# Kernel optimization log

Measured on AMD Instinct MI355X. Metric: run time of the kernel, lower is better.

The kernel has to match this reference:

```python
import jax, jax.numpy as jnp
import numpy as np
import math

B, T, C, H = 2, 2048, 768, 12
HD = C // H
EPS = 1e-5

def setup_inputs() -> dict:
    key = jax.random.key(0)
    ks = jax.random.split(key, 12)
    s = lambda n: 1.0 / math.sqrt(n)
    return {
        "x": jax.random.normal(ks[0], (B, T, C), jnp.float32),
        "ln1_g": jnp.ones((C,), jnp.float32),
        "ln1_b": jnp.zeros((C,), jnp.float32),
        "w_attn": jax.random.normal(ks[1], (C, 3 * C), jnp.float32) * s(C),
        "b_attn": jnp.zeros((3 * C,), jnp.float32),
        "w_proj": jax.random.normal(ks[2], (C, C), jnp.float32) * s(C),
        "b_proj": jnp.zeros((C,), jnp.float32),
        "ln2_g": jnp.ones((C,), jnp.float32),
        "ln2_b": jnp.zeros((C,), jnp.float32),
        "w_fc": jax.random.normal(ks[3], (C, 4 * C), jnp.float32) * s(C),
        "b_fc": jnp.zeros((4 * C,), jnp.float32),
        "w_fc2": jax.random.normal(ks[4], (4 * C, C), jnp.float32) * s(4 * C),
        "b_fc2": jnp.zeros((C,), jnp.float32),
    }

def layernorm(x, g, b):
    mu = jnp.mean(x, axis=-1, keepdims=True)
    var = jnp.mean(jnp.square(x - mu), axis=-1, keepdims=True)
    return (x - mu) * jax.lax.rsqrt(var + EPS) * g + b

def new_gelu(x):
    c = math.sqrt(2.0 / math.pi)
    return 0.5 * x * (1.0 + jnp.tanh(c * (x + 0.044715 * x ** 3)))

def reference(x, ln1_g, ln1_b, w_attn, b_attn, w_proj, b_proj,
              ln2_g, ln2_b, w_fc, b_fc, w_fc2, b_fc2):
    # --- attention branch ---
    h = layernorm(x, ln1_g, ln1_b)
    qkv = h @ w_attn + b_attn                       # [B,T,3C]
    q, k, v = jnp.split(qkv, 3, axis=-1)
    q = q.reshape(B, T, H, HD).transpose(0, 2, 1, 3)  # [B,H,T,hd]
    k = k.reshape(B, T, H, HD).transpose(0, 2, 1, 3)
    v = v.reshape(B, T, H, HD).transpose(0, 2, 1, 3)
    att = jnp.einsum('bhqd,bhkd->bhqk', q, k) * (1.0 / math.sqrt(HD))
    causal = jnp.tril(jnp.ones((T, T), bool))
    att = jnp.where(causal, att, -jnp.inf)
    att = jax.nn.softmax(att, axis=-1)
    y = jnp.einsum('bhqk,bhkd->bhqd', att, v)       # [B,H,T,hd]
    y = y.transpose(0, 2, 1, 3).reshape(B, T, C)
    x = x + y @ w_proj + b_proj
    # --- MLP branch ---
    h2 = layernorm(x, ln2_g, ln2_b)
    x = x + new_gelu(h2 @ w_fc + b_fc) @ w_fc2 + b_fc2
    return x
```

## Files before the change

kernel.cpp:

```cpp
#include <hip/hip_runtime.h>
#include <hip/hip_bf16.h>
#include <math.h>

typedef __hip_bfloat16 bf16;
typedef __attribute__((ext_vector_type(8))) short short8;
typedef __attribute__((ext_vector_type(4))) float floatx4;
typedef __attribute__((ext_vector_type(4))) unsigned uintx4;

#define GLDS16(g, l) __builtin_amdgcn_global_load_lds( \
    (const __attribute__((address_space(1))) void*)(g), \
    (__attribute__((address_space(3))) void*)(l), 16, 0, 0)

__device__ __forceinline__ bf16 f2bf(float v) { return __float2bfloat16(v); }

__device__ __forceinline__ unsigned cvtpk(float a, float b) {
  unsigned r;
  asm volatile("v_cvt_pk_bf16_f32 %0, %1, %2" : "=v"(r) : "v"(a), "v"(b));
  return r;
}

__global__ __launch_bounds__(256) void kconvT(const float* __restrict__ w,
                                              bf16* __restrict__ wT,
                                              int K, int N) {
  __shared__ float tile[32][33];
  const int n0 = blockIdx.x * 32, k0 = blockIdx.y * 32;
  const int tc = threadIdx.x & 31, tr = threadIdx.x >> 5;
#pragma unroll
  for (int p = 0; p < 4; p++)
    tile[tr + p * 8][tc] = w[(size_t)(k0 + tr + p * 8) * N + n0 + tc];
  __syncthreads();
#pragma unroll
  for (int p = 0; p < 4; p++)
    wT[(size_t)(n0 + tr + p * 8) * K + k0 + tc] = f2bf(tile[tc][tr + p * 8]);
}

__global__ __launch_bounds__(256) void kln(const float* __restrict__ x,
                                           const float* __restrict__ gw,
                                           const float* __restrict__ bw,
                                           bf16* __restrict__ out) {
  const int row = blockIdx.x, tid = threadIdx.x;
  const float* xr = x + (size_t)row * 768;
  float v0 = xr[tid], v1 = xr[tid + 256], v2 = xr[tid + 512];
  float s = v0 + v1 + v2;
  float s2 = v0 * v0 + v1 * v1 + v2 * v2;
#pragma unroll
  for (int off = 1; off < 64; off <<= 1) {
    s += __shfl_xor(s, off);
    s2 += __shfl_xor(s2, off);
  }
  __shared__ float red[8];
  const int wid = tid >> 6, lane = tid & 63;
  if (lane == 0) { red[wid] = s; red[4 + wid] = s2; }
  __syncthreads();
  s = red[0] + red[1] + red[2] + red[3];
  s2 = red[4] + red[5] + red[6] + red[7];
  const float mu = s * (1.f / 768.f);
  const float rst = rsqrtf(fmaxf(s2 * (1.f / 768.f) - mu * mu, 0.f) + 1e-5f);
  bf16* orow = out + (size_t)row * 768;
  orow[tid] = f2bf((v0 - mu) * rst * gw[tid] + bw[tid]);
  orow[tid + 256] = f2bf((v1 - mu) * rst * gw[tid + 256] + bw[tid + 256]);
  orow[tid + 512] = f2bf((v2 - mu) * rst * gw[tid + 512] + bw[tid + 512]);
}

__global__ __launch_bounds__(256) void kxpose(const bf16* __restrict__ qkv,
                                              bf16* __restrict__ VT) {
  const int T = 2048, C3 = 2304;
  const int t0 = blockIdx.x * 64, h = blockIdx.y, b = blockIdx.z;
  const int tid = threadIdx.x;
  __shared__ short tile[64][66];
  const bf16* src = qkv + (size_t)b * T * C3 + 1536 + h * 64;
  const int tr = tid >> 3, c = tid & 7;
#pragma unroll
  for (int p = 0; p < 2; p++) {
    short8 v = *(const short8*)(src + (size_t)(t0 + tr + p * 32) * C3 + c * 8);
    *(short8*)&tile[tr + p * 32][c * 8] = v;
  }
  __syncthreads();
  bf16* dst = VT + ((size_t)(b * 12 + h) * 64) * T + t0;
#pragma unroll
  for (int p = 0; p < 2; p++) {
    const int d = (tid >> 3) + p * 32, tc = tid & 7;
    short8 v;
#pragma unroll
    for (int j = 0; j < 8; j++) v[j] = tile[tc * 8 + j][d];
    *(short8*)(dst + (size_t)d * T + tc * 8) = v;
  }
}

template <int BN, int EPI>
__global__ __launch_bounds__(256, 2) void kgemm(
    const bf16* __restrict__ A, const bf16* __restrict__ BT,
    const float* __restrict__ bias, const float* __restrict__ resid,
    bf16* __restrict__ outb, float* __restrict__ outf, int M, int N, int K,
    int NXB) {
  __shared__ bf16 As[3][128 * 32];
  __shared__ bf16 Bs[3][BN * 32];
  const int tid = threadIdx.x;
  const int wid = tid >> 6, lane = tid & 63, g = lane >> 4, q = lane & 15;
  constexpr int FM = (BN == 128) ? 4 : 2;
  constexpr int FN = 4;
  constexpr int WM = (BN == 128) ? 64 : 32;
  const int wr = (BN == 128) ? (wid >> 1) : wid;
  const int wc = (BN == 128) ? (wid & 1) : 0;

  const int bid = blockIdx.x;
  const int lb = (bid & 7) * ((int)gridDim.x >> 3) + (bid >> 3);
  const int row0 = (lb / NXB) * 128, col0 = (lb % NXB) * BN;

  floatx4 acc[FM][FN] = {};
  const int r0 = tid >> 2;
  const int c0 = (((tid & 3) ^ ((r0 >> 1) & 3))) * 8;
  const int lsl = (g ^ ((q >> 1) & 3)) * 16;
  const bf16* Ab = A + (size_t)row0 * K;
  const bf16* Bb = BT + (size_t)col0 * K;

  auto STAGE = [&](int kk, int buf) {
    GLDS16(Ab + (size_t)r0 * K + kk + c0, (char*)&As[buf][0] + wid * 1024);
    GLDS16(Ab + (size_t)(r0 + 64) * K + kk + c0,
           (char*)&As[buf][0] + 4096 + wid * 1024);
    GLDS16(Bb + (size_t)r0 * K + kk + c0, (char*)&Bs[buf][0] + wid * 1024);
    if constexpr (BN == 128)
      GLDS16(Bb + (size_t)(r0 + 64) * K + kk + c0,
             (char*)&Bs[buf][0] + 4096 + wid * 1024);
  };

  const int nk = K >> 5;
  STAGE(0, 0);
  STAGE(32, 1);

  for (int kt = 0; kt < nk; kt++) {
    if (kt + 2 < nk) {
      STAGE((kt + 2) << 5, (kt + 2) % 3);
      if constexpr (BN == 128) asm volatile("s_waitcnt vmcnt(8)");
      else asm volatile("s_waitcnt vmcnt(6)");
    } else if (kt + 1 < nk) {
      if constexpr (BN == 128) asm volatile("s_waitcnt vmcnt(4)");
      else asm volatile("s_waitcnt vmcnt(3)");
    } else {
      asm volatile("s_waitcnt vmcnt(0)");
    }
    __syncthreads();

    const char* Ac = (const char*)&As[kt % 3][0];
    const char* Bc = (const char*)&Bs[kt % 3][0];
    short8 af[FM], bfr[FN];
#pragma unroll
    for (int m = 0; m < FM; m++)
      af[m] = *(const short8*)(Ac + (wr * WM + m * 16 + q) * 64 + lsl);
#pragma unroll
    for (int n = 0; n < FN; n++)
      bfr[n] = *(const short8*)(Bc + (wc * 64 + n * 16 + q) * 64 + lsl);
#pragma unroll
    for (int m = 0; m < FM; m++)
#pragma unroll
      for (int n = 0; n < FN; n++)
        acc[m][n] =
            __builtin_amdgcn_mfma_f32_16x16x32_bf16(af[m], bfr[n], acc[m][n], 0, 0, 0);
    __syncthreads();
  }

#pragma unroll
  for (int n = 0; n < FN; n++) {
    const int col = col0 + wc * 64 + n * 16 + q;
    const float bv = bias[col];
#pragma unroll
    for (int m = 0; m < FM; m++) {
      const int rowb = row0 + wr * WM + m * 16 + g * 4;
#pragma unroll
      for (int r = 0; r < 4; r++) {
        const size_t idx = (size_t)(rowb + r) * N + col;
        const float v = acc[m][n][r] + bv;
        if (EPI == 0) {
          outb[idx] = f2bf(v);
        } else if (EPI == 1) {
          outf[idx] = v + resid[idx];
        } else {
          const float t = tanhf(0.7978845608028654f * (v + 0.044715f * v * v * v));
          outb[idx] = f2bf(0.5f * v * (1.0f + t));
        }
      }
    }
  }
}

__global__ __launch_bounds__(256, 2) void kattn(const bf16* __restrict__ qkv,
                                                const bf16* __restrict__ VT,
                                                bf16* __restrict__ y) {
  const int T = 2048, C3 = 2304;
  const int tid = threadIdx.x;
  const int w = tid >> 6, lane = tid & 63;
  const int g = lane >> 4, qi = lane & 15;

  const int bid = blockIdx.x;
  const int lb = (bid & 7) * 96 + (bid >> 3);
  const int qblk = 31 - (lb & 31);
  const int h = (lb >> 5) % 12, b = (lb >> 5) / 12;
  const int q0w = qblk * 64 + w * 16;
  const int qrow = q0w + qi;

  const bf16* Qb = qkv + (size_t)b * T * C3 + h * 64;
  const char* Ksrc = (const char*)(Qb + 768);
  const char* Vsrc = (const char*)(VT + (size_t)(b * 12 + h) * 64 * T);

  __shared__ __align__(16) char smem[32768];

  const int nt = qblk + 1;

  short8 qf[2];
#pragma unroll
  for (int s = 0; s < 2; s++)
    qf[s] = *(const short8*)(Qb + (size_t)qrow * C3 + s * 32 + g * 8);

  const int kvb = (qi >> 2) * 8 + (qi & 3);
  const unsigned swz = (unsigned)(((lane & 7) ^ (lane >> 3)) << 4);
  const int srow = lane >> 3;

  float m_run = -1e30f, l_run = 0.f;
  floatx4 o[4] = {};

#define STAGE(t)                                                                   \
  {                                                                                \
    char* base_ = smem + ((t) & 1) * 16384;                                        \
    const int kv0_ = (t) * 64;                                                     \
    _Pragma("unroll")                                                              \
    for (int j = 0; j < 2; j++) {                                                  \
      const int c_ = w * 2 + j;                                                    \
      GLDS16(Ksrc + (size_t)(kv0_ + c_ * 8 + srow) * 4608 + swz, base_ + c_ * 1024); \
      GLDS16(Vsrc + (size_t)(c_ * 8 + srow) * 4096 + kv0_ * 2 + swz,               \
             base_ + 8192 + c_ * 1024);                                            \
    }                                                                              \
  }

  STAGE(0);
  asm volatile("s_waitcnt vmcnt(0)");
  __syncthreads();

  for (int t = 0; t < nt; t++) {
    if (t + 1 < nt) STAGE(t + 1);
    const char* Kl = smem + (t & 1) * 16384;
    const char* Vl = Kl + 8192;
    const int kv0 = t * 64;

    short8 kf[8];
#pragma unroll
    for (int c = 0; c < 4; c++) {
      const int R = kvb + (c & 1) * 4 + (c >> 1) * 32;
#pragma unroll
      for (int s = 0; s < 2; s++)
        kf[c * 2 + s] =
            *(const short8*)(Kl + R * 128 + (((s * 4 + g) ^ (R & 7)) << 4));
    }
    short8 vfr[8];
#pragma unroll
    for (int ks = 0; ks < 2; ks++)
#pragma unroll
      for (int n = 0; n < 4; n++) {
        const int R2 = n * 16 + qi;
        vfr[ks * 4 + n] =
            *(const short8*)(Vl + R2 * 128 + (((ks * 4 + g) ^ (R2 & 7)) << 4));
      }

    floatx4 sacc[4] = {};
#pragma unroll
    for (int c = 0; c < 4; c++)
#pragma unroll
      for (int s = 0; s < 2; s++)
        sacc[c] =
            __builtin_amdgcn_mfma_f32_16x16x32_bf16(kf[c * 2 + s], qf[s], sacc[c], 0, 0, 0);

    if (kv0 + 63 > q0w) {
#pragma unroll
      for (int c = 0; c < 4; c++)
#pragma unroll
        for (int r = 0; r < 4; r++) {
          const int kv = kv0 + g * 8 + (c & 1) * 4 + r + (c >> 1) * 32;
          if (kv > qrow) sacc[c][r] = -1e30f;
        }
    }
    float mx = sacc[0][0];
#pragma unroll
    for (int c = 0; c < 4; c++)
#pragma unroll
      for (int r = 0; r < 4; r++) mx = fmaxf(mx, sacc[c][r]);
    mx = fmaxf(mx, __shfl_xor(mx, 16));
    mx = fmaxf(mx, __shfl_xor(mx, 32));
    mx *= 0.125f;
    const float mn = fmaxf(m_run, mx);
    const float al = __expf(m_run - mn);
    float ps = 0.f;
    unsigned pk[8];
#pragma unroll
    for (int c = 0; c < 4; c++) {
      float p0 = __expf(fmaf(sacc[c][0], 0.125f, -mn));
      float p1 = __expf(fmaf(sacc[c][1], 0.125f, -mn));
      float p2 = __expf(fmaf(sacc[c][2], 0.125f, -mn));
      float p3 = __expf(fmaf(sacc[c][3], 0.125f, -mn));
      ps += (p0 + p1) + (p2 + p3);
      pk[c * 2] = cvtpk(p0, p1);
      pk[c * 2 + 1] = cvtpk(p2, p3);
    }
    ps += __shfl_xor(ps, 16);
    ps += __shfl_xor(ps, 32);
    l_run = l_run * al + ps;
    m_run = mn;
#pragma unroll
    for (int n = 0; n < 4; n++) o[n] *= al;

#pragma unroll
    for (int ks = 0; ks < 2; ks++) {
      uintx4 pu;
      pu.x = pk[ks * 4 + 0];
      pu.y = pk[ks * 4 + 1];
      pu.z = pk[ks * 4 + 2];
      pu.w = pk[ks * 4 + 3];
      const short8 pf = __builtin_bit_cast(short8, pu);
#pragma unroll
      for (int n = 0; n < 4; n++)
        o[n] = __builtin_amdgcn_mfma_f32_16x16x32_bf16(vfr[ks * 4 + n], pf, o[n], 0, 0, 0);
    }

    asm volatile("s_waitcnt vmcnt(0)");
    __syncthreads();
  }
#undef STAGE

  const float inv = 1.0f / l_run;
  bf16* yr = y + (size_t)(b * T + qrow) * 768 + h * 64;
#pragma unroll
  for (int n = 0; n < 4; n++) {
    uint2 pr;
    pr.x = cvtpk(o[n][0] * inv, o[n][1] * inv);
    pr.y = cvtpk(o[n][2] * inv, o[n][3] * inv);
    *(uint2*)(yr + n * 16 + g * 4) = pr;
  }
}

extern "C" void kernel_launch(void* const* d_in, const int* in_sizes, int n_in,
                              void* d_out, int out_size, void* d_ws, size_t ws_size,
                              hipStream_t stream) {
  const float* x      = (const float*)d_in[0];
  const float* ln1_g  = (const float*)d_in[1];
  const float* ln1_b  = (const float*)d_in[2];
  const float* w_attn = (const float*)d_in[3];
  const float* b_attn = (const float*)d_in[4];
  const float* w_proj = (const float*)d_in[5];
  const float* b_proj = (const float*)d_in[6];
  const float* ln2_g  = (const float*)d_in[7];
  const float* ln2_b  = (const float*)d_in[8];
  const float* w_fc   = (const float*)d_in[9];
  const float* b_fc   = (const float*)d_in[10];
  const float* w_fc2  = (const float*)d_in[11];
  const float* b_fc2  = (const float*)d_in[12];
  float* out = (float*)d_out;

  const int M = 4096;
  char* p = (char*)d_ws;
  bf16* wT_attn = (bf16*)p; p += (size_t)2304 * 768 * 2;
  bf16* wT_proj = (bf16*)p; p += (size_t)768 * 768 * 2;
  bf16* wT_fc   = (bf16*)p; p += (size_t)3072 * 768 * 2;
  bf16* wT_fc2  = (bf16*)p; p += (size_t)768 * 3072 * 2;
  bf16* h       = (bf16*)p; p += (size_t)M * 768 * 2;
  bf16* qkv     = (bf16*)p;
  bf16* yb      = (bf16*)(p + (size_t)M * 2304 * 2);
  bf16* act     = qkv;      p += (size_t)M * 2304 * 2 + (size_t)M * 768 * 2;
  float* x1     = (float*)p;
  bf16* VT      = (bf16*)p;

  kconvT<<<dim3(2304 / 32, 768 / 32), 256, 0, stream>>>(w_attn, wT_attn, 768, 2304);
  kconvT<<<dim3(768 / 32, 768 / 32), 256, 0, stream>>>(w_proj, wT_proj, 768, 768);
  kconvT<<<dim3(3072 / 32, 768 / 32), 256, 0, stream>>>(w_fc, wT_fc, 768, 3072);
  kconvT<<<dim3(768 / 32, 3072 / 32), 256, 0, stream>>>(w_fc2, wT_fc2, 3072, 768);

  kln<<<M, 256, 0, stream>>>(x, ln1_g, ln1_b, h);
  kgemm<128, 0><<<dim3(18 * 32), 256, 0, stream>>>(
      h, wT_attn, b_attn, nullptr, qkv, nullptr, M, 2304, 768, 18);
  kxpose<<<dim3(32, 12, 2), 256, 0, stream>>>(qkv, VT);
  kattn<<<dim3(768), 256, 0, stream>>>(qkv, VT, yb);
  kgemm<64, 1><<<dim3(12 * 32), 256, 0, stream>>>(
      yb, wT_proj, b_proj, x, nullptr, x1, M, 768, 768, 12);

  kln<<<M, 256, 0, stream>>>(x1, ln2_g, ln2_b, h);
  kgemm<128, 2><<<dim3(24 * 32), 256, 0, stream>>>(
      h, wT_fc, b_fc, nullptr, act, nullptr, M, 3072, 768, 24);
  kgemm<64, 1><<<dim3(12 * 32), 256, 0, stream>>>(
      act, wT_fc2, b_fc2, x1, nullptr, out, M, 768, 3072, 12);
}
```

Before: 211.1 us.

## Split-K the N=768 projection GEMMs with atomic accumulation into pre-initialized output

```diff
diff --git a/kernel.cpp b/kernel.cpp
--- a/kernel.cpp
+++ b/kernel.cpp
@@ -85,6 +85,15 @@
     for (int j = 0; j < 8; j++) v[j] = tile[tc * 8 + j][d];
     *(short8*)(dst + (size_t)d * T + tc * 8) = v;
   }
+}
+
+__global__ __launch_bounds__(256) void kinit(const float* __restrict__ resid,
+                                             const float* __restrict__ bias,
+                                             float* __restrict__ out, int N) {
+  const size_t i4 = ((size_t)blockIdx.x * 256 + threadIdx.x) * 4;
+  const floatx4 r = *(const floatx4*)(resid + i4);
+  const floatx4 bv = *(const floatx4*)(bias + (i4 % N));
+  *(floatx4*)(out + i4) = r + bv;
 }
 
 template <int BN, int EPI>
@@ -172,12 +181,91 @@
         const float v = acc[m][n][r] + bv;
         if (EPI == 0) {
           outb[idx] = f2bf(v);
-        } else if (EPI == 1) {
-          outf[idx] = v + resid[idx];
         } else {
           const float t = tanhf(0.7978845608028654f * (v + 0.044715f * v * v * v));
           outb[idx] = f2bf(0.5f * v * (1.0f + t));
         }
+      }
+    }
+  }
+}
+
+template <int BN>
+__global__ __launch_bounds__(256, 2) void kgemmsk(
+    const bf16* __restrict__ A, const bf16* __restrict__ BT,
+    float* __restrict__ outf, int M, int N, int K, int NXB, int TILES,
+    int KSL) {
+  __shared__ bf16 As[3][128 * 32];
+  __shared__ bf16 Bs[3][BN * 32];
+  const int tid = threadIdx.x;
+  const int wid = tid >> 6, lane = tid & 63, g = lane >> 4, q = lane & 15;
+  constexpr int FM = 2;
+  constexpr int FN = 4;
+  constexpr int WM = 32;
+  const int wr = wid, wc = 0;
+
+  const int bid = blockIdx.x;
+  const int lb = (bid & 7) * ((int)gridDim.x >> 3) + (bid >> 3);
+  const int ks = lb / TILES, t = lb % TILES;
+  const int row0 = (t / NXB) * 128, col0 = (t % NXB) * BN;
+
+  floatx4 acc[FM][FN] = {};
+  const int r0 = tid >> 2;
+  const int c0 = (((tid & 3) ^ ((r0 >> 1) & 3))) * 8;
+  const int lsl = (g ^ ((q >> 1) & 3)) * 16;
+  const bf16* Ab = A + (size_t)row0 * K + ks * KSL;
+  const bf16* Bb = BT + (size_t)col0 * K + ks * KSL;
+
+  auto STAGE = [&](int kk, int buf) {
+    GLDS16(Ab + (size_t)r0 * K + kk + c0, (char*)&As[buf][0] + wid * 1024);
+    GLDS16(Ab + (size_t)(r0 + 64) * K + kk + c0,
+           (char*)&As[buf][0] + 4096 + wid * 1024);
+    GLDS16(Bb + (size_t)r0 * K + kk + c0, (char*)&Bs[buf][0] + wid * 1024);
+  };
+
+  const int nk = KSL >> 5;
+  STAGE(0, 0);
+  STAGE(32, 1);
+
+  for (int kt = 0; kt < nk; kt++) {
+    if (kt + 2 < nk) {
+      STAGE((kt + 2) << 5, (kt + 2) % 3);
+      asm volatile("s_waitcnt vmcnt(6)");
+    } else if (kt + 1 < nk) {
+      asm volatile("s_waitcnt vmcnt(3)");
+    } else {
+      asm volatile("s_waitcnt vmcnt(0)");
+    }
+    __syncthreads();
+
+    const char* Ac = (const char*)&As[kt % 3][0];
+    const char* Bc = (const char*)&Bs[kt % 3][0];
+    short8 af[FM], bfr[FN];
+#pragma unroll
+    for (int m = 0; m < FM; m++)
+      af[m] = *(const short8*)(Ac + (wr * WM + m * 16 + q) * 64 + lsl);
+#pragma unroll
+    for (int n = 0; n < FN; n++)
+      bfr[n] = *(const short8*)(Bc + (wc * 64 + n * 16 + q) * 64 + lsl);
+#pragma unroll
+    for (int m = 0; m < FM; m++)
+#pragma unroll
+      for (int n = 0; n < FN; n++)
+        acc[m][n] =
+            __builtin_amdgcn_mfma_f32_16x16x32_bf16(af[m], bfr[n], acc[m][n], 0, 0, 0);
+    __syncthreads();
+  }
+
+#pragma unroll
+  for (int n = 0; n < FN; n++) {
+    const int col = col0 + wc * 64 + n * 16 + q;
+#pragma unroll
+    for (int m = 0; m < FM; m++) {
+      const int rowb = row0 + wr * WM + m * 16 + g * 4;
+#pragma unroll
+      for (int r = 0; r < 4; r++) {
+        const size_t idx = (size_t)(rowb + r) * N + col;
+        unsafeAtomicAdd(&outf[idx], acc[m][n][r]);
       }
     }
   }
@@ -376,12 +464,14 @@
       h, wT_attn, b_attn, nullptr, qkv, nullptr, M, 2304, 768, 18);
   kxpose<<<dim3(32, 12, 2), 256, 0, stream>>>(qkv, VT);
   kattn<<<dim3(768), 256, 0, stream>>>(qkv, VT, yb);
-  kgemm<64, 1><<<dim3(12 * 32), 256, 0, stream>>>(
-      yb, wT_proj, b_proj, x, nullptr, x1, M, 768, 768, 12);
+  kinit<<<dim3(M * 768 / 1024), 256, 0, stream>>>(x, b_proj, x1, 768);
+  kgemmsk<64><<<dim3(768), 256, 0, stream>>>(
+      yb, wT_proj, x1, M, 768, 768, 12, 384, 384);
 
   kln<<<M, 256, 0, stream>>>(x1, ln2_g, ln2_b, h);
   kgemm<128, 2><<<dim3(24 * 32), 256, 0, stream>>>(
       h, wT_fc, b_fc, nullptr, act, nullptr, M, 3072, 768, 24);
-  kgemm<64, 1><<<dim3(12 * 32), 256, 0, stream>>>(
-      act, wT_fc2, b_fc2, x1, nullptr, out, M, 768, 3072, 12);
-}
+  kinit<<<dim3(M * 768 / 1024), 256, 0, stream>>>(x1, b_fc2, out, 768);
+  kgemmsk<64><<<dim3(1536), 256, 0, stream>>>(
+      act, wT_fc2, out, M, 768, 3072, 12, 384, 768);
+}
```

Result: slower. 247.2 us (+17.1%).
